# Kernel optimization log

Measured on AMD Instinct MI355X. Metric: run time of the kernel, lower is better.

Reference implementation:

```python
import jax, jax.numpy as jnp
import numpy as np

SENSOR_DIM = 256
MODEL_DIM = 512
NUM_DATASETS = 8


def setup_inputs() -> dict:
    key = jax.random.key(0)
    k1, k2, k3 = jax.random.split(key, 3)
    x = jax.random.normal(k1, (32, 200, 1024), dtype=jnp.float32)
    dataset_id = jax.random.randint(k2, (32,), 0, NUM_DATASETS)
    # Conv1d weight [out_ch, in_ch, k] and bias, as in torch.nn.Conv1d
    W = jax.random.normal(k3, (NUM_DATASETS * MODEL_DIM, SENSOR_DIM, 3), dtype=jnp.float32) * 0.02
    b = jnp.zeros((NUM_DATASETS * MODEL_DIM,), dtype=jnp.float32)
    return {"x": x, "dataset_id": dataset_id, "W": W, "b": b}


def reference(x, dataset_id, W, b):
    B, c_in, T = x.shape
    # DatasetPadding: zero-pad channel dim up to sensor_dim
    if c_in < SENSOR_DIM:
        x = jnp.pad(x, ((0, 0), (0, SENSOR_DIM - c_in), (0, 0)))
    # Conv1d(sensor_dim -> num_datasets*model_dim, kernel=3, padding=1)
    y = jax.lax.conv_general_dilated(
        x, W, window_strides=(1,), padding=((1, 1),),
        dimension_numbers=("NCH", "OIH", "NCH"))
    y = y + b[None, :, None]
    y = jax.nn.gelu(y, approximate=False)  # torch GELU default = exact erf
    # unflatten channels to (num_datasets, model_dim) and select per-example dataset slice
    y = y.reshape(B, NUM_DATASETS, MODEL_DIM, T)
    onehot = jax.nn.one_hot(dataset_id, NUM_DATASETS, dtype=y.dtype)  # [B, D]
    out = jnp.einsum("bdmt,bd->bmt", y, onehot)  # [B, model_dim, T]
    return out
```

## Files before the change

kernel.cpp:

```cpp
#include <hip/hip_runtime.h>


typedef unsigned short u16;
typedef __attribute__((ext_vector_type(8))) short bf16x8;
typedef __attribute__((ext_vector_type(4))) float f32x4;

#define CIN 200
#define CINP 224
#define T 1024
#define BATCH 32
#define MD 512
#define XT_ROWS 1026
#define NCHUNK 7
#define XP_PITCH 202

__device__ __forceinline__ u16 f2bf(float f) {
    unsigned u = __float_as_uint(f);
    u += 0x7FFFu + ((u >> 16) & 1u);
    return (u16)(u >> 16);
}

__device__ __forceinline__ void g2l16(void* lds, const void* g) {
    __builtin_amdgcn_global_load_lds(
        (const __attribute__((address_space(1))) unsigned int*)(uintptr_t)g,
        (__attribute__((address_space(3))) unsigned int*)(unsigned)(uintptr_t)lds,
        16, 0, 0);
}

__global__ __launch_bounds__(256) void prep(const float* __restrict__ x,
                                            const float* __restrict__ W,
                                            u16* __restrict__ xt,
                                            u16* __restrict__ wt) {
    __shared__ u16 tile[64 * XP_PITCH];
    const int tid = threadIdx.x;
    if (blockIdx.x < 512) {
        const int b  = blockIdx.x >> 4;
        const int bx = blockIdx.x & 15;
        const int t0 = bx * 64;
        const int tl = tid & 63;
        const int w  = tid >> 6;
        const float* xb = x + (size_t)b * CIN * T + t0 + tl;
        for (int i = w; i < CIN; i += 4)
            tile[tl * XP_PITCH + i] = f2bf(xb[(size_t)i * T]);
        __syncthreads();
        u16* xrow = xt + ((size_t)b * XT_ROWS + 1 + t0) * CINP;
        for (int it = 0; it < 16; ++it) {
            int r = it * 4 + w;
            if (tl < 56) {
                ushort4 v = {0, 0, 0, 0};
                if (tl < 50) {
                    const u16* p = tile + r * XP_PITCH + tl * 4;
                    v.x = p[0]; v.y = p[1]; v.z = p[2]; v.w = p[3];
                }
                *(ushort4*)(xrow + (size_t)r * CINP + tl * 4) = v;
            }
        }
        if (bx == 0 && tid < 112)
            ((unsigned*)(xt + (size_t)b * XT_ROWS * CINP))[tid] = 0;
        if (bx == 15 && tid < 112)
            ((unsigned*)(xt + ((size_t)b * XT_ROWS + 1025) * CINP))[tid] = 0;
    } else {
        int idx = (blockIdx.x - 512) * 256 + tid;
        int o = idx / CINP;
        int i = idx - o * CINP;
        const float* wp = W + (size_t)o * 768 + i * 3;
        u16* wo = wt + (size_t)o * 3 * CINP + i;
        float w0 = wp[0], w1 = wp[1], w2 = wp[2];
        wo[0]        = f2bf(w0);
        wo[CINP]     = f2bf(w1);
        wo[2 * CINP] = f2bf(w2);
    }
}

__global__ __launch_bounds__(256) void conv_mfma(const u16* __restrict__ xt,
                                                 const u16* __restrict__ wt,
                                                 const int* __restrict__ dsid,
                                                 const float* __restrict__ bias,
                                                 float* __restrict__ out) {
    __shared__ __align__(16) u16 xs[520 * 8];
    __shared__ __align__(16) u16 wsm[1536 * 8];

    const int tid = threadIdx.x;
    const int wave = tid >> 6, lane = tid & 63;
    const int l = lane & 15, quad = lane >> 4;
    const int wm  = (wave & 1) * 64;
    const int wti = (wave >> 1) * 64;

    const int t0 = blockIdx.x * 128;
    const int m0 = blockIdx.y * 128;
    const int b  = blockIdx.z;
    const int d  = dsid[b];
    const int obase = d * MD + m0;

    f32x4 acc[4][4];
#pragma unroll
    for (int mi = 0; mi < 4; ++mi)
#pragma unroll
        for (int ti = 0; ti < 4; ++ti) acc[mi][ti] = (f32x4){0.f, 0.f, 0.f, 0.f};

    const u16* xbase = xt + ((size_t)b * XT_ROWS + t0) * CINP;
    const u16* wbase = wt + (size_t)obase * 3 * CINP;

    for (int c = 0; c < NCHUNK; ++c) {
        const int ic = c * 32;
        for (int g = tid; g < 520; g += 256) {
            int r = g >> 2, p = g & 3, s = p ^ (r & 3);
            g2l16(xs + (size_t)(g & ~63) * 8, xbase + (size_t)r * CINP + ic + s * 8);
        }
        for (int g = tid; g < 1536; g += 256) {
            int p = g & 3, m = (g >> 2) & 127, k = g >> 9;
            int s = p ^ (m & 3);
            g2l16(wsm + (size_t)(g & ~63) * 8, wbase + ((size_t)m * 3 + k) * CINP + ic + s * 8);
        }
        __syncthreads();

#pragma unroll
        for (int tap = 0; tap < 3; ++tap) {
            bf16x8 a[4];
#pragma unroll
            for (int mi = 0; mi < 4; ++mi) {
                int mr = tap * 128 + wm + mi * 16 + l;
                a[mi] = *(const bf16x8*)(wsm + ((size_t)mr * 4 + (quad ^ (l & 3))) * 8);
            }
#pragma unroll
            for (int ti = 0; ti < 4; ++ti) {
                int row = wti + ti * 16 + l + tap;
                bf16x8 bv = *(const bf16x8*)(xs + ((size_t)row * 4 + (quad ^ (row & 3))) * 8);
#pragma unroll
                for (int mi = 0; mi < 4; ++mi)
                    acc[mi][ti] = __builtin_amdgcn_mfma_f32_16x16x32_bf16(a[mi], bv, acc[mi][ti], 0, 0, 0);
            }
        }
        __syncthreads();
    }

#pragma unroll
    for (int mi = 0; mi < 4; ++mi) {
        float bv[4];
#pragma unroll
        for (int r = 0; r < 4; ++r)
            bv[r] = bias[obase + wm + mi * 16 + quad * 4 + r];
#pragma unroll
        for (int ti = 0; ti < 4; ++ti) {
            int t = t0 + wti + ti * 16 + l;
#pragma unroll
            for (int r = 0; r < 4; ++r) {
                int m = wm + mi * 16 + quad * 4 + r;
                float v = acc[mi][ti][r] + bv[r];
                float p2 = v * v;
                float z = v * fmaf(p2, 0.07135481283f, 1.5957691216f);
                float e = __expf(-z);
                float g = v * __builtin_amdgcn_rcpf(1.0f + e);
                out[((size_t)(b * MD + m0 + m)) * T + t] = g;
            }
        }
    }
}

extern "C" void kernel_launch(void* const* d_in, const int* in_sizes, int n_in,
                              void* d_out, int out_size, void* d_ws, size_t ws_size,
                              hipStream_t stream) {
    const float* x    = (const float*)d_in[0];
    const int*   dsid = (const int*)d_in[1];
    const float* W    = (const float*)d_in[2];
    const float* bias = (const float*)d_in[3];
    float* out = (float*)d_out;

    u16* xt = (u16*)d_ws;
    u16* wt = xt + (size_t)BATCH * XT_ROWS * CINP;

    prep<<<512 + 3584, 256, 0, stream>>>(x, W, xt, wt);
    conv_mfma<<<dim3(8, 4, BATCH), 256, 0, stream>>>(xt, wt, dsid, bias, out);
}
```

Before: 132.7 us.

## Widen conv time tile to 256, swizzle block order, precompute load addresses

Each conv block now covers 256 timesteps instead of 128, so every wave holds an 8x4 grid of MFMA accumulators. This halves the grid to 512 blocks and the number of times weights are reloaded per time range. Block indices are remapped so that blocks sharing a batch and time range are adjacent, which favours cache reuse, and the global-to-LDS source and destination addresses are computed once outside the channel loop. The GELU exponential is folded into a base-2 exp2 with prescaled constants. Register pressure and LDS per block rise, so launch bounds now request 2 blocks per SM, with a risk of spills or lower occupancy.

Measured after the change: 124.4 us. 1.07x faster.

```diff
diff --git a/kernel.cpp b/kernel.cpp
--- a/kernel.cpp
+++ b/kernel.cpp
@@ -13,6 +13,10 @@
 #define XT_ROWS 1026
 #define NCHUNK 7
 #define XP_PITCH 202
+#define TT 256
+#define XROWS (TT + 2)
+#define XGRAN (XROWS * 4)
+#define WGRAN 1536
 
 __device__ __forceinline__ u16 f2bf(float f) {
     unsigned u = __float_as_uint(f);
@@ -72,46 +76,63 @@
     }
 }
 
-__global__ __launch_bounds__(256) void conv_mfma(const u16* __restrict__ xt,
-                                                 const u16* __restrict__ wt,
-                                                 const int* __restrict__ dsid,
-                                                 const float* __restrict__ bias,
-                                                 float* __restrict__ out) {
-    __shared__ __align__(16) u16 xs[520 * 8];
-    __shared__ __align__(16) u16 wsm[1536 * 8];
+__global__ __launch_bounds__(256, 2) void conv_mfma(const u16* __restrict__ xt,
+                                                    const u16* __restrict__ wt,
+                                                    const int* __restrict__ dsid,
+                                                    const float* __restrict__ bias,
+                                                    float* __restrict__ out) {
+    __shared__ __align__(16) u16 xs[XGRAN * 8];
+    __shared__ __align__(16) u16 wsm[WGRAN * 8];
 
     const int tid = threadIdx.x;
     const int wave = tid >> 6, lane = tid & 63;
     const int l = lane & 15, quad = lane >> 4;
     const int wm  = (wave & 1) * 64;
-    const int wti = (wave >> 1) * 64;
+    const int wti = (wave >> 1) * 128;
 
-    const int t0 = blockIdx.x * 128;
-    const int m0 = blockIdx.y * 128;
-    const int b  = blockIdx.z;
+    const int id = blockIdx.x;
+    const int tb = (id >> 5) * 8 + (id & 7);
+    const int m0 = ((id >> 3) & 3) * 128;
+    const int t0 = (tb & 3) * TT;
+    const int b  = tb >> 2;
     const int d  = dsid[b];
     const int obase = d * MD + m0;
 
-    f32x4 acc[4][4];
+    f32x4 acc[4][8];
 #pragma unroll
     for (int mi = 0; mi < 4; ++mi)
 #pragma unroll
-        for (int ti = 0; ti < 4; ++ti) acc[mi][ti] = (f32x4){0.f, 0.f, 0.f, 0.f};
+        for (int ti = 0; ti < 8; ++ti) acc[mi][ti] = (f32x4){0.f, 0.f, 0.f, 0.f};
 
     const u16* xbase = xt + ((size_t)b * XT_ROWS + t0) * CINP;
     const u16* wbase = wt + (size_t)obase * 3 * CINP;
 
+    const u16* xsrc[5]; u16* xdst[5];
+#pragma unroll
+    for (int k = 0; k < 5; ++k) {
+        int g = tid + k * 256;
+        int r = g >> 2, p = g & 3, s = p ^ (r & 3);
+        if (g < XGRAN) { xsrc[k] = xbase + (size_t)r * CINP + s * 8; xdst[k] = xs + (size_t)(g & ~63) * 8; }
+        else           { xsrc[k] = xbase;                            xdst[k] = xs; }
+    }
+    const u16* wsrc[6]; u16* wdst[6];
+#pragma unroll
+    for (int k = 0; k < 6; ++k) {
+        int g = tid + k * 256;
+        int p = g & 3, m = (g >> 2) & 127, kk = g >> 9;
+        int s = p ^ (m & 3);
+        wsrc[k] = wbase + ((size_t)m * 3 + kk) * CINP + s * 8;
+        wdst[k] = wsm + (size_t)(g & ~63) * 8;
+    }
+
     for (int c = 0; c < NCHUNK; ++c) {
         const int ic = c * 32;
-        for (int g = tid; g < 520; g += 256) {
-            int r = g >> 2, p = g & 3, s = p ^ (r & 3);
-            g2l16(xs + (size_t)(g & ~63) * 8, xbase + (size_t)r * CINP + ic + s * 8);
-        }
-        for (int g = tid; g < 1536; g += 256) {
-            int p = g & 3, m = (g >> 2) & 127, k = g >> 9;
-            int s = p ^ (m & 3);
-            g2l16(wsm + (size_t)(g & ~63) * 8, wbase + ((size_t)m * 3 + k) * CINP + ic + s * 8);
-        }
+#pragma unroll
+        for (int k = 0; k < 5; ++k)
+            if (tid + k * 256 < XGRAN) g2l16(xdst[k], xsrc[k] + ic);
+#pragma unroll
+        for (int k = 0; k < 6; ++k)
+            g2l16(wdst[k], wsrc[k] + ic);
         __syncthreads();
 
 #pragma unroll
@@ -123,7 +144,7 @@
                 a[mi] = *(const bf16x8*)(wsm + ((size_t)mr * 4 + (quad ^ (l & 3))) * 8);
             }
 #pragma unroll
-            for (int ti = 0; ti < 4; ++ti) {
+            for (int ti = 0; ti < 8; ++ti) {
                 int row = wti + ti * 16 + l + tap;
                 bf16x8 bv = *(const bf16x8*)(xs + ((size_t)row * 4 + (quad ^ (row & 3))) * 8);
 #pragma unroll
@@ -141,15 +162,15 @@
         for (int r = 0; r < 4; ++r)
             bv[r] = bias[obase + wm + mi * 16 + quad * 4 + r];
 #pragma unroll
-        for (int ti = 0; ti < 4; ++ti) {
+        for (int ti = 0; ti < 8; ++ti) {
             int t = t0 + wti + ti * 16 + l;
 #pragma unroll
             for (int r = 0; r < 4; ++r) {
                 int m = wm + mi * 16 + quad * 4 + r;
                 float v = acc[mi][ti][r] + bv[r];
                 float p2 = v * v;
-                float z = v * fmaf(p2, 0.07135481283f, 1.5957691216f);
-                float e = __expf(-z);
+                float z2 = v * fmaf(p2, -0.10295089f, -2.30243665f);
+                float e = __builtin_amdgcn_exp2f(z2);
                 float g = v * __builtin_amdgcn_rcpf(1.0f + e);
                 out[((size_t)(b * MD + m0 + m)) * T + t] = g;
             }
@@ -170,5 +191,5 @@
     u16* wt = xt + (size_t)BATCH * XT_ROWS * CINP;
 
     prep<<<512 + 3584, 256, 0, stream>>>(x, W, xt, wt);
-    conv_mfma<<<dim3(8, 4, BATCH), 256, 0, stream>>>(xt, wt, dsid, bias, out);
+    conv_mfma<<<512, 256, 0, stream>>>(xt, wt, dsid, bias, out);
 }
```
